# Kernel optimization log

Measured on AMD Instinct MI355X. Metric: run time of the kernel, lower is better.

Reference implementation:

```python
import jax, jax.numpy as jnp
import numpy as np

N_NODES = 100000
N_EDGES = 1600000
IN_DIM = 64
OUT_DIM = 64
BN_EPS = 1e-5


def batchnorm(h, gamma, beta):
    # BatchNorm1d in training mode: per-feature batch stats, biased variance
    mean = jnp.mean(h, axis=0)
    var = jnp.mean((h - mean) ** 2, axis=0)
    return gamma * (h - mean) * jax.lax.rsqrt(var + BN_EPS) + beta


def setup_inputs() -> dict:
    key = jax.random.key(0)
    ks = jax.random.split(key, 4)
    x = jax.random.normal(ks[0], (N_NODES, IN_DIM), dtype=jnp.float32)
    edge_index = jax.random.randint(ks[1], (2, N_EDGES), 0, N_NODES, dtype=jnp.int32)
    epsilon = jnp.asarray(0.1, dtype=jnp.float32)
    # Linear weights stored [in, out] (transpose of torch layout)
    W1 = jax.random.normal(ks[2], (IN_DIM, 2 * OUT_DIM), dtype=jnp.float32) * (1.0 / np.sqrt(IN_DIM))
    b1 = jnp.zeros((2 * OUT_DIM,), dtype=jnp.float32)
    g1 = jnp.ones((2 * OUT_DIM,), dtype=jnp.float32)
    be1 = jnp.zeros((2 * OUT_DIM,), dtype=jnp.float32)
    W2 = jax.random.normal(ks[3], (2 * OUT_DIM, OUT_DIM), dtype=jnp.float32) * (1.0 / np.sqrt(2 * OUT_DIM))
    b2 = jnp.zeros((OUT_DIM,), dtype=jnp.float32)
    g2 = jnp.ones((OUT_DIM,), dtype=jnp.float32)
    be2 = jnp.zeros((OUT_DIM,), dtype=jnp.float32)
    return {"x": x, "edge_index": edge_index, "epsilon": epsilon,
            "W1": W1, "b1": b1, "g1": g1, "be1": be1,
            "W2": W2, "b2": b2, "g2": g2, "be2": be2}


def reference(x, edge_index, epsilon, W1, b1, g1, be1, W2, b2, g2, be2):
    src, dst = edge_index[0], edge_index[1]
    # gather messages from src, scatter-add into dst  [N, D]
    neighbor_sum = jnp.zeros_like(x).at[dst].add(x[src])
    combined = (1.0 + epsilon) * x + neighbor_sum
    h = combined @ W1 + b1            # [N, 2*out_dim]
    h = jax.nn.relu(batchnorm(h, g1, be1))
    h = h @ W2 + b2                   # [N, out_dim]
    return batchnorm(h, g2, be2)
```

## Files before the change

kernel.cpp:

```cpp
#include <hip/hip_runtime.h>

#define N_NODES 100000
#define N_EDGES 1600000
#define IN_DIM 64
#define H_DIM 128
#define OUT_DIM 64
#define BN_EPS 1e-5f
#define CAP 64
#define BIN_SHIFT 9
#define BIN_NODES 512
#define NB 256
#define BINCAP 10240
#define NBIN_BLOCKS ((N_NODES + BIN_NODES - 1) / BIN_NODES)

#define OFF_XB     0
#define OFF_SRCL   3200000
#define OFF_BINNED 9600000
#define OFF_COMB   15000000
#define OFF_H1     18200000
#define OFF_H2     24600000
#define OFF_CNT    27800000
#define OFF_STATS  28000000
#define S1SUM 0
#define S1SQ  128
#define S2SUM 256
#define S2SQ  320

#define DEV_ATOMIC_ADD(p, v) __hip_atomic_fetch_add((p), (v), __ATOMIC_RELAXED, __HIP_MEMORY_SCOPE_AGENT)

typedef __attribute__((ext_vector_type(8))) short short8;
typedef __attribute__((ext_vector_type(4))) float f32x4;

__device__ __forceinline__ unsigned short f2bf(float f) {
  union { float f; unsigned u; } v; v.f = f;
  unsigned r = v.u + 0x7FFFu + ((v.u >> 16) & 1u);
  return (unsigned short)(r >> 16);
}
__device__ __forceinline__ float bflo(unsigned v) { union { unsigned u; float f; } t; t.u = v << 16; return t.f; }
__device__ __forceinline__ float bfhi(unsigned v) { union { unsigned u; float f; } t; t.u = v & 0xFFFF0000u; return t.f; }

__device__ __forceinline__ void acc8(float* a, uint4 v) {
  a[0] += bflo(v.x); a[1] += bfhi(v.x); a[2] += bflo(v.y); a[3] += bfhi(v.y);
  a[4] += bflo(v.z); a[5] += bfhi(v.z); a[6] += bflo(v.w); a[7] += bfhi(v.w);
}
__device__ __forceinline__ uint4 pack8(const float* a) {
  uint4 o;
  o.x = (unsigned)f2bf(a[0]) | ((unsigned)f2bf(a[1]) << 16);
  o.y = (unsigned)f2bf(a[2]) | ((unsigned)f2bf(a[3]) << 16);
  o.z = (unsigned)f2bf(a[4]) | ((unsigned)f2bf(a[5]) << 16);
  o.w = (unsigned)f2bf(a[6]) | ((unsigned)f2bf(a[7]) << 16);
  return o;
}

__global__ __launch_bounds__(256) void k_bsplit(const float* __restrict__ x,
                                                unsigned short* __restrict__ xb,
                                                const int* __restrict__ ei,
                                                int* __restrict__ bcnt,
                                                int2* __restrict__ binned) {
  __shared__ int lcnt[NB];
  __shared__ int lbase[NB];
  const int tid = threadIdx.x;
  lcnt[tid] = 0;
  #pragma unroll
  for (int j = 0; j < 8; ++j) {
    int i = blockIdx.x * 2048 + j * 256 + tid;
    if (i < N_NODES * IN_DIM / 4) {
      float4 v = ((const float4*)x)[i];
      ushort4 o;
      o.x = f2bf(v.x); o.y = f2bf(v.y); o.z = f2bf(v.z); o.w = f2bf(v.w);
      *(ushort4*)(xb + i * 4) = o;
    }
  }
  __syncthreads();
  int src[8], dst[8], rk[8];
  #pragma unroll
  for (int j = 0; j < 8; ++j) {
    int e = blockIdx.x * 2048 + j * 256 + tid;
    if (e < N_EDGES) {
      src[j] = ei[e];
      dst[j] = ei[N_EDGES + e];
      rk[j] = atomicAdd(&lcnt[dst[j] >> BIN_SHIFT], 1);
    } else {
      src[j] = -1;
    }
  }
  __syncthreads();
  if (lcnt[tid] > 0) lbase[tid] = DEV_ATOMIC_ADD(&bcnt[tid], lcnt[tid]);
  __syncthreads();
  #pragma unroll
  for (int j = 0; j < 8; ++j) {
    if (src[j] >= 0) {
      int b = dst[j] >> BIN_SHIFT;
      int pos = lbase[b] + rk[j];
      if (pos < BINCAP) binned[b * BINCAP + pos] = make_int2(src[j], dst[j]);
    }
  }
}

__global__ __launch_bounds__(512) void k_bfill(const int* __restrict__ bcnt,
                                               const int2* __restrict__ binned,
                                               int* __restrict__ cnt,
                                               int* __restrict__ srcl) {
  __shared__ int lcnt[BIN_NODES];
  const int tid = threadIdx.x;
  for (int i = tid; i < BIN_NODES; i += 512) lcnt[i] = 0;
  __syncthreads();
  const int b = blockIdx.x;
  int n = bcnt[b];
  if (n > BINCAP) n = BINCAP;
  const int2* run = binned + b * BINCAP;
  const int base = b * BIN_NODES;
  for (int i = tid; i < n; i += 512) {
    int2 ed = run[i];
    int pos = atomicAdd(&lcnt[ed.y - base], 1);
    if (pos < CAP) srcl[ed.y * CAP + pos] = ed.x;
  }
  __syncthreads();
  for (int i = tid; i < BIN_NODES; i += 512) {
    int node = base + i;
    if (node < N_NODES) cnt[node] = lcnt[i];
  }
}

__global__ __launch_bounds__(256, 5) void k_gather(const unsigned short* __restrict__ xb,
                                                   const float* __restrict__ eps,
                                                   const int* __restrict__ cnt,
                                                   const int* __restrict__ srcl,
                                                   unsigned short* __restrict__ comb) {
  const int t = blockIdx.x * 256 + threadIdx.x;
  const int node = t >> 3;
  const int sub = t & 7;
  if (node >= N_NODES) return;

  float a[8];
  {
    uint4 sv = *(const uint4*)(xb + node * 64 + sub * 8);
    float e1 = 1.0f + eps[0];
    a[0] = bflo(sv.x) * e1; a[1] = bfhi(sv.x) * e1;
    a[2] = bflo(sv.y) * e1; a[3] = bfhi(sv.y) * e1;
    a[4] = bflo(sv.z) * e1; a[5] = bfhi(sv.z) * e1;
    a[6] = bflo(sv.w) * e1; a[7] = bfhi(sv.w) * e1;
  }
  int deg = cnt[node];
  if (deg > CAP) deg = CAP;
  const int* sl = srcl + node * CAP;

  uint4 n0 = *(const uint4*)sl;
  uint4 n1 = *(const uint4*)(sl + 4);
  int j = 0;
  while (j + 8 <= deg) {
    uint4 i0 = n0, i1 = n1;
    uint4 r0 = *(const uint4*)(xb + (size_t)i0.x * 64 + sub * 8);
    uint4 r1 = *(const uint4*)(xb + (size_t)i0.y * 64 + sub * 8);
    uint4 r2 = *(const uint4*)(xb + (size_t)i0.z * 64 + sub * 8);
    uint4 r3 = *(const uint4*)(xb + (size_t)i0.w * 64 + sub * 8);
    uint4 r4 = *(const uint4*)(xb + (size_t)i1.x * 64 + sub * 8);
    uint4 r5 = *(const uint4*)(xb + (size_t)i1.y * 64 + sub * 8);
    uint4 r6 = *(const uint4*)(xb + (size_t)i1.z * 64 + sub * 8);
    uint4 r7 = *(const uint4*)(xb + (size_t)i1.w * 64 + sub * 8);
    j += 8;
    n0 = *(const uint4*)(sl + j);
    n1 = *(const uint4*)(sl + j + 4);
    acc8(a, r0); acc8(a, r1); acc8(a, r2); acc8(a, r3);
    acc8(a, r4); acc8(a, r5); acc8(a, r6); acc8(a, r7);
  }
  if (j + 4 <= deg) {
    uint4 i0 = *(const uint4*)(sl + j);
    uint4 r0 = *(const uint4*)(xb + (size_t)i0.x * 64 + sub * 8);
    uint4 r1 = *(const uint4*)(xb + (size_t)i0.y * 64 + sub * 8);
    uint4 r2 = *(const uint4*)(xb + (size_t)i0.z * 64 + sub * 8);
    uint4 r3 = *(const uint4*)(xb + (size_t)i0.w * 64 + sub * 8);
    acc8(a, r0); acc8(a, r1); acc8(a, r2); acc8(a, r3);
    j += 4;
  }
  if (j + 2 <= deg) {
    int2 i2 = *(const int2*)(sl + j);
    uint4 r0 = *(const uint4*)(xb + (size_t)i2.x * 64 + sub * 8);
    uint4 r1 = *(const uint4*)(xb + (size_t)i2.y * 64 + sub * 8);
    acc8(a, r0); acc8(a, r1);
    j += 2;
  }
  if (j < deg) {
    int s0 = sl[j];
    uint4 r0 = *(const uint4*)(xb + (size_t)s0 * 64 + sub * 8);
    acc8(a, r0);
  }
  *(uint4*)(comb + node * 64 + sub * 8) = pack8(a);
}

#define APAD 72
__global__ __launch_bounds__(256) void k_gemm1(const unsigned short* __restrict__ comb,
                                               const float* __restrict__ W1,
                                               const float* __restrict__ b1,
                                               unsigned short* __restrict__ h1,
                                               float* __restrict__ stats) {
  __shared__ unsigned short As[128 * APAD];
  __shared__ unsigned short Ws[128 * APAD];
  __shared__ float red[4][128];
  const int tid = threadIdx.x;
  const int wv = tid >> 6, lane = tid & 63;
  const int quad = lane >> 4, ln = lane & 15;
  const int rowBase = blockIdx.x * 128;

  #pragma unroll
  for (int it = 0; it < 8; ++it) {
    int idx = it * 256 + tid;
    int k = idx >> 5, n4 = idx & 31;
    float4 wv1 = *(const float4*)(W1 + k * 128 + n4 * 4);
    Ws[(n4 * 4 + 0) * APAD + k] = f2bf(wv1.x);
    Ws[(n4 * 4 + 1) * APAD + k] = f2bf(wv1.y);
    Ws[(n4 * 4 + 2) * APAD + k] = f2bf(wv1.z);
    Ws[(n4 * 4 + 3) * APAD + k] = f2bf(wv1.w);
  }
  #pragma unroll
  for (int it = 0; it < 4; ++it) {
    int idx = it * 256 + tid;
    int row = idx >> 3, ch = idx & 7;
    int g = rowBase * 8 + idx;
    uint4 u = (g < N_NODES * 8) ? ((const uint4*)comb)[g] : make_uint4(0, 0, 0, 0);
    *(uint4*)&As[row * APAD + ch * 8] = u;
  }
  __syncthreads();

  f32x4 acc[2][8];
  #pragma unroll
  for (int mt = 0; mt < 2; ++mt) {
    #pragma unroll
    for (int nt = 0; nt < 8; ++nt) acc[mt][nt] = (f32x4)0.0f;
  }
  const int rw = wv * 32;
  #pragma unroll
  for (int kb = 0; kb < 2; ++kb) {
    short8 a0 = *(short8*)&As[(rw + ln) * APAD + kb * 32 + quad * 8];
    short8 a1 = *(short8*)&As[(rw + 16 + ln) * APAD + kb * 32 + quad * 8];
    #pragma unroll
    for (int nt = 0; nt < 8; ++nt) {
      short8 b = *(short8*)&Ws[(nt * 16 + ln) * APAD + kb * 32 + quad * 8];
      acc[0][nt] = __builtin_amdgcn_mfma_f32_16x16x32_bf16(a0, b, acc[0][nt], 0, 0, 0);
      acc[1][nt] = __builtin_amdgcn_mfma_f32_16x16x32_bf16(a1, b, acc[1][nt], 0, 0, 0);
    }
  }

  float bias[8], s[8], q[8];
  #pragma unroll
  for (int nt = 0; nt < 8; ++nt) { bias[nt] = b1[nt * 16 + ln]; s[nt] = 0.f; q[nt] = 0.f; }
  #pragma unroll
  for (int mt = 0; mt < 2; ++mt) {
    #pragma unroll
    for (int i = 0; i < 4; ++i) {
      int gRow = rowBase + rw + mt * 16 + quad * 4 + i;
      if (gRow < N_NODES) {
        #pragma unroll
        for (int nt = 0; nt < 8; ++nt) {
          float v = acc[mt][nt][i] + bias[nt];
          h1[gRow * 128 + nt * 16 + ln] = f2bf(v);
          s[nt] += v; q[nt] += v * v;
        }
      }
    }
  }
  #pragma unroll
  for (int nt = 0; nt < 8; ++nt) {
    s[nt] += __shfl_xor(s[nt], 16); s[nt] += __shfl_xor(s[nt], 32);
    q[nt] += __shfl_xor(q[nt], 16); q[nt] += __shfl_xor(q[nt], 32);
  }
  if (lane < 16) {
    #pragma unroll
    for (int nt = 0; nt < 8; ++nt) red[wv][nt * 16 + ln] = s[nt];
  }
  __syncthreads();
  if (tid < 128) DEV_ATOMIC_ADD(&stats[S1SUM + tid],
                                red[0][tid] + red[1][tid] + red[2][tid] + red[3][tid]);
  __syncthreads();
  if (lane < 16) {
    #pragma unroll
    for (int nt = 0; nt < 8; ++nt) red[wv][nt * 16 + ln] = q[nt];
  }
  __syncthreads();
  if (tid < 128) DEV_ATOMIC_ADD(&stats[S1SQ + tid],
                                red[0][tid] + red[1][tid] + red[2][tid] + red[3][tid]);
}

#define WPAD 136
__global__ __launch_bounds__(256) void k_gemm2(const unsigned short* __restrict__ h1,
                                               const float* __restrict__ W2,
                                               const float* __restrict__ b2,
                                               const float* __restrict__ g1,
                                               const float* __restrict__ be1,
                                               unsigned short* __restrict__ h2,
                                               float* __restrict__ stats) {
  __shared__ unsigned short As[128 * APAD];
  __shared__ unsigned short Ws[64 * WPAD];
  __shared__ float red[4][64];
  __shared__ float scL[128], shL[128];
  const int tid = threadIdx.x;
  const int wv = tid >> 6, lane = tid & 63;
  const int quad = lane >> 4, ln = lane & 15;
  const int rowBase = blockIdx.x * 128;

  if (tid < 128) {
    float mean = stats[S1SUM + tid] * (1.0f / N_NODES);
    float var = stats[S1SQ + tid] * (1.0f / N_NODES) - mean * mean;
    var = fmaxf(var, 0.0f);
    float sc = g1[tid] * rsqrtf(var + BN_EPS);
    scL[tid] = sc;
    shL[tid] = be1[tid] - mean * sc;
  }
  #pragma unroll
  for (int it = 0; it < 8; ++it) {
    int idx = it * 256 + tid;
    int k = idx >> 4, n4 = idx & 15;
    float4 wv2 = *(const float4*)(W2 + k * 64 + n4 * 4);
    Ws[(n4 * 4 + 0) * WPAD + k] = f2bf(wv2.x);
    Ws[(n4 * 4 + 1) * WPAD + k] = f2bf(wv2.y);
    Ws[(n4 * 4 + 2) * WPAD + k] = f2bf(wv2.z);
    Ws[(n4 * 4 + 3) * WPAD + k] = f2bf(wv2.w);
  }

  f32x4 acc[2][4];
  #pragma unroll
  for (int mt = 0; mt < 2; ++mt) {
    #pragma unroll
    for (int nt = 0; nt < 4; ++nt) acc[mt][nt] = (f32x4)0.0f;
  }
  const int rw = wv * 32;

  for (int kc = 0; kc < 2; ++kc) {
    __syncthreads();
    #pragma unroll
    for (int it = 0; it < 4; ++it) {
      int idx = it * 256 + tid;
      int row = idx >> 3, ch = idx & 7;
      int gRow = rowBase + row;
      uint4 u = (gRow < N_NODES) ? *(const uint4*)(h1 + gRow * 128 + kc * 64 + ch * 8)
                                 : make_uint4(0, 0, 0, 0);
      int kb = kc * 64 + ch * 8;
      float f0 = fmaxf(bflo(u.x) * scL[kb + 0] + shL[kb + 0], 0.f);
      float f1 = fmaxf(bfhi(u.x) * scL[kb + 1] + shL[kb + 1], 0.f);
      float f2 = fmaxf(bflo(u.y) * scL[kb + 2] + shL[kb + 2], 0.f);
      float f3 = fmaxf(bfhi(u.y) * scL[kb + 3] + shL[kb + 3], 0.f);
      float f4 = fmaxf(bflo(u.z) * scL[kb + 4] + shL[kb + 4], 0.f);
      float f5 = fmaxf(bfhi(u.z) * scL[kb + 5] + shL[kb + 5], 0.f);
      float f6 = fmaxf(bflo(u.w) * scL[kb + 6] + shL[kb + 6], 0.f);
      float f7 = fmaxf(bfhi(u.w) * scL[kb + 7] + shL[kb + 7], 0.f);
      uint4 o;
      o.x = (unsigned)f2bf(f0) | ((unsigned)f2bf(f1) << 16);
      o.y = (unsigned)f2bf(f2) | ((unsigned)f2bf(f3) << 16);
      o.z = (unsigned)f2bf(f4) | ((unsigned)f2bf(f5) << 16);
      o.w = (unsigned)f2bf(f6) | ((unsigned)f2bf(f7) << 16);
      *(uint4*)&As[row * APAD + ch * 8] = o;
    }
    __syncthreads();
    #pragma unroll
    for (int kb = 0; kb < 2; ++kb) {
      short8 a0 = *(short8*)&As[(rw + ln) * APAD + kb * 32 + quad * 8];
      short8 a1 = *(short8*)&As[(rw + 16 + ln) * APAD + kb * 32 + quad * 8];
      #pragma unroll
      for (int nt = 0; nt < 4; ++nt) {
        short8 b = *(short8*)&Ws[(nt * 16 + ln) * WPAD + kc * 64 + kb * 32 + quad * 8];
        acc[0][nt] = __builtin_amdgcn_mfma_f32_16x16x32_bf16(a0, b, acc[0][nt], 0, 0, 0);
        acc[1][nt] = __builtin_amdgcn_mfma_f32_16x16x32_bf16(a1, b, acc[1][nt], 0, 0, 0);
      }
    }
  }

  float bias[4], s[4], q[4];
  #pragma unroll
  for (int nt = 0; nt < 4; ++nt) { bias[nt] = b2[nt * 16 + ln]; s[nt] = 0.f; q[nt] = 0.f; }
  #pragma unroll
  for (int mt = 0; mt < 2; ++mt) {
    #pragma unroll
    for (int i = 0; i < 4; ++i) {
      int gRow = rowBase + rw + mt * 16 + quad * 4 + i;
      if (gRow < N_NODES) {
        #pragma unroll
        for (int nt = 0; nt < 4; ++nt) {
          float v = acc[mt][nt][i] + bias[nt];
          h2[gRow * 64 + nt * 16 + ln] = f2bf(v);
          s[nt] += v; q[nt] += v * v;
        }
      }
    }
  }
  #pragma unroll
  for (int nt = 0; nt < 4; ++nt) {
    s[nt] += __shfl_xor(s[nt], 16); s[nt] += __shfl_xor(s[nt], 32);
    q[nt] += __shfl_xor(q[nt], 16); q[nt] += __shfl_xor(q[nt], 32);
  }
  if (lane < 16) {
    #pragma unroll
    for (int nt = 0; nt < 4; ++nt) red[wv][nt * 16 + ln] = s[nt];
  }
  __syncthreads();
  if (tid < 64) DEV_ATOMIC_ADD(&stats[S2SUM + tid],
                               red[0][tid] + red[1][tid] + red[2][tid] + red[3][tid]);
  __syncthreads();
  if (lane < 16) {
    #pragma unroll
    for (int nt = 0; nt < 4; ++nt) red[wv][nt * 16 + ln] = q[nt];
  }
  __syncthreads();
  if (tid < 64) DEV_ATOMIC_ADD(&stats[S2SQ + tid],
                               red[0][tid] + red[1][tid] + red[2][tid] + red[3][tid]);
}

__global__ __launch_bounds__(256) void k_out(const unsigned short* __restrict__ h2,
                                             const float* __restrict__ stats,
                                             const float* __restrict__ g2,
                                             const float* __restrict__ be2,
                                             float* __restrict__ out) {
  __shared__ float scL[64], shL[64];
  const int tid = threadIdx.x;
  if (tid < 64) {
    float mean = stats[S2SUM + tid] * (1.0f / N_NODES);
    float var = stats[S2SQ + tid] * (1.0f / N_NODES) - mean * mean;
    var = fmaxf(var, 0.0f);
    float sc = g2[tid] * rsqrtf(var + BN_EPS);
    scL[tid] = sc;
    shL[tid] = be2[tid] - mean * sc;
  }
  __syncthreads();
  int i = blockIdx.x * 256 + tid;
  if (i < N_NODES * OUT_DIM / 4) {
    int c = i & 15;
    uint2 u = *(const uint2*)(h2 + i * 4);
    float4 v = {bflo(u.x), bfhi(u.x), bflo(u.y), bfhi(u.y)};
    float4 sc = ((const float4*)scL)[c];
    float4 sh = ((const float4*)shL)[c];
    v.x = v.x * sc.x + sh.x;
    v.y = v.y * sc.y + sh.y;
    v.z = v.z * sc.z + sh.z;
    v.w = v.w * sc.w + sh.w;
    ((float4*)out)[i] = v;
  }
}

extern "C" void kernel_launch(void* const* d_in, const int* in_sizes, int n_in,
                              void* d_out, int out_size, void* d_ws, size_t ws_size,
                              hipStream_t stream) {
  const float* x   = (const float*)d_in[0];
  const int*   ei  = (const int*)d_in[1];
  const float* eps = (const float*)d_in[2];
  const float* W1  = (const float*)d_in[3];
  const float* b1  = (const float*)d_in[4];
  const float* g1  = (const float*)d_in[5];
  const float* be1 = (const float*)d_in[6];
  const float* W2  = (const float*)d_in[7];
  const float* b2  = (const float*)d_in[8];
  const float* g2  = (const float*)d_in[9];
  const float* be2 = (const float*)d_in[10];

  float* ws = (float*)d_ws;
  unsigned short* xb     = (unsigned short*)(ws + OFF_XB);
  int*            srcl   = (int*)(ws + OFF_SRCL);
  int2*           binned = (int2*)(ws + OFF_BINNED);
  unsigned short* comb   = (unsigned short*)(ws + OFF_COMB);
  unsigned short* h1     = (unsigned short*)(ws + OFF_H1);
  unsigned short* h2     = (unsigned short*)(ws + OFF_H2);
  int*            cnt    = (int*)(ws + OFF_CNT);
  float*          stats  = ws + OFF_STATS;
  int*            bcnt   = (int*)(stats + 768);
  float*          out    = (float*)d_out;

  hipMemsetAsync(stats, 0, 1024 * sizeof(float), stream);

  const int edgeGrid = (N_EDGES + 2047) / 2048;
  const int gemmGrid = (N_NODES + 127) / 128;
  const int gatherGrid = (N_NODES * 8 + 255) / 256;
  k_bsplit<<<edgeGrid, 256, 0, stream>>>(x, xb, ei, bcnt, binned);
  k_bfill<<<NBIN_BLOCKS, 512, 0, stream>>>(bcnt, binned, cnt, srcl);
  k_gather<<<gatherGrid, 256, 0, stream>>>(xb, eps, cnt, srcl, comb);
  k_gemm1<<<gemmGrid, 256, 0, stream>>>(comb, W1, b1, h1, stats);
  k_gemm2<<<gemmGrid, 256, 0, stream>>>(h1, W2, b2, g1, be1, h2, stats);
  k_out<<<(N_NODES * OUT_DIM / 4 + 255) / 256, 256, 0, stream>>>(h2, stats, g2, be2, out);
}
```

Measured before the change: 239.2 us.

## Replace binned two-pass adjacency build with direct global atomic fill

Removes the bin-split and bin-fill kernels that staged edges by destination bucket using shared-memory atomics. Edges are now inserted directly into per-node source lists using device-scope atomic counters on a zeroed count array. This drops one kernel launch and the intermediate binned edge buffer, but replaces local atomics and grouped writes with random global atomics and scattered stores. It also adds a memset for the count array.

```diff
diff --git a/kernel.cpp b/kernel.cpp
--- a/kernel.cpp
+++ b/kernel.cpp
@@ -7,20 +7,14 @@
 #define OUT_DIM 64
 #define BN_EPS 1e-5f
 #define CAP 64
-#define BIN_SHIFT 9
-#define BIN_NODES 512
-#define NB 256
-#define BINCAP 10240
-#define NBIN_BLOCKS ((N_NODES + BIN_NODES - 1) / BIN_NODES)
 
 #define OFF_XB     0
 #define OFF_SRCL   3200000
-#define OFF_BINNED 9600000
-#define OFF_COMB   15000000
-#define OFF_H1     18200000
-#define OFF_H2     24600000
-#define OFF_CNT    27800000
-#define OFF_STATS  28000000
+#define OFF_COMB   9600000
+#define OFF_H1     12800000
+#define OFF_H2     19200000
+#define OFF_CNT    22400000
+#define OFF_STATS  22600000
 #define S1SUM 0
 #define S1SQ  128
 #define S2SUM 256
@@ -52,15 +46,12 @@
   return o;
 }
 
-__global__ __launch_bounds__(256) void k_bsplit(const float* __restrict__ x,
-                                                unsigned short* __restrict__ xb,
-                                                const int* __restrict__ ei,
-                                                int* __restrict__ bcnt,
-                                                int2* __restrict__ binned) {
-  __shared__ int lcnt[NB];
-  __shared__ int lbase[NB];
+__global__ __launch_bounds__(256) void k_build(const float* __restrict__ x,
+                                               unsigned short* __restrict__ xb,
+                                               const int* __restrict__ ei,
+                                               int* __restrict__ cnt,
+                                               int* __restrict__ srcl) {
   const int tid = threadIdx.x;
-  lcnt[tid] = 0;
   #pragma unroll
   for (int j = 0; j < 8; ++j) {
     int i = blockIdx.x * 2048 + j * 256 + tid;
@@ -71,54 +62,15 @@
       *(ushort4*)(xb + i * 4) = o;
     }
   }
-  __syncthreads();
-  int src[8], dst[8], rk[8];
   #pragma unroll
   for (int j = 0; j < 8; ++j) {
     int e = blockIdx.x * 2048 + j * 256 + tid;
     if (e < N_EDGES) {
-      src[j] = ei[e];
-      dst[j] = ei[N_EDGES + e];
-      rk[j] = atomicAdd(&lcnt[dst[j] >> BIN_SHIFT], 1);
-    } else {
-      src[j] = -1;
-    }
-  }
-  __syncthreads();
-  if (lcnt[tid] > 0) lbase[tid] = DEV_ATOMIC_ADD(&bcnt[tid], lcnt[tid]);
-  __syncthreads();
-  #pragma unroll
-  for (int j = 0; j < 8; ++j) {
-    if (src[j] >= 0) {
-      int b = dst[j] >> BIN_SHIFT;
-      int pos = lbase[b] + rk[j];
-      if (pos < BINCAP) binned[b * BINCAP + pos] = make_int2(src[j], dst[j]);
-    }
-  }
-}
-
-__global__ __launch_bounds__(512) void k_bfill(const int* __restrict__ bcnt,
-                                               const int2* __restrict__ binned,
-                                               int* __restrict__ cnt,
-                                               int* __restrict__ srcl) {
-  __shared__ int lcnt[BIN_NODES];
-  const int tid = threadIdx.x;
-  for (int i = tid; i < BIN_NODES; i += 512) lcnt[i] = 0;
-  __syncthreads();
-  const int b = blockIdx.x;
-  int n = bcnt[b];
-  if (n > BINCAP) n = BINCAP;
-  const int2* run = binned + b * BINCAP;
-  const int base = b * BIN_NODES;
-  for (int i = tid; i < n; i += 512) {
-    int2 ed = run[i];
-    int pos = atomicAdd(&lcnt[ed.y - base], 1);
-    if (pos < CAP) srcl[ed.y * CAP + pos] = ed.x;
-  }
-  __syncthreads();
-  for (int i = tid; i < BIN_NODES; i += 512) {
-    int node = base + i;
-    if (node < N_NODES) cnt[node] = lcnt[i];
+      int src = ei[e];
+      int dst = ei[N_EDGES + e];
+      int pos = DEV_ATOMIC_ADD(&cnt[dst], 1);
+      if (pos < CAP) srcl[dst * CAP + pos] = src;
+    }
   }
 }
 
@@ -453,22 +405,20 @@
   float* ws = (float*)d_ws;
   unsigned short* xb     = (unsigned short*)(ws + OFF_XB);
   int*            srcl   = (int*)(ws + OFF_SRCL);
-  int2*           binned = (int2*)(ws + OFF_BINNED);
   unsigned short* comb   = (unsigned short*)(ws + OFF_COMB);
   unsigned short* h1     = (unsigned short*)(ws + OFF_H1);
   unsigned short* h2     = (unsigned short*)(ws + OFF_H2);
   int*            cnt    = (int*)(ws + OFF_CNT);
   float*          stats  = ws + OFF_STATS;
-  int*            bcnt   = (int*)(stats + 768);
   float*          out    = (float*)d_out;
 
-  hipMemsetAsync(stats, 0, 1024 * sizeof(float), stream);
+  hipMemsetAsync(stats, 0, 768 * sizeof(float), stream);
+  hipMemsetAsync(cnt, 0, N_NODES * sizeof(int), stream);
 
   const int edgeGrid = (N_EDGES + 2047) / 2048;
   const int gemmGrid = (N_NODES + 127) / 128;
   const int gatherGrid = (N_NODES * 8 + 255) / 256;
-  k_bsplit<<<edgeGrid, 256, 0, stream>>>(x, xb, ei, bcnt, binned);
-  k_bfill<<<NBIN_BLOCKS, 512, 0, stream>>>(bcnt, binned, cnt, srcl);
+  k_build<<<edgeGrid, 256, 0, stream>>>(x, xb, ei, cnt, srcl);
   k_gather<<<gatherGrid, 256, 0, stream>>>(xb, eps, cnt, srcl, comb);
   k_gemm1<<<gemmGrid, 256, 0, stream>>>(comb, W1, b1, h1, stats);
   k_gemm2<<<gemmGrid, 256, 0, stream>>>(h1, W2, b2, g1, be1, h2, stats);
```

New measurement: 335.2 us. 40.1% more time.

## Pack binned edges into single ints and split gather across two thread groups

Applied to the files above, without the earlier changes.

Binned edge records shrink from int2 (src, dst) to a single packed int holding the source index and the local destination offset, which halves the binning write and read traffic. The gather kernel now gives each node 16 threads in two groups that take alternating 4-edge chunks and combine their partial sums with a cross-lane shuffle. This doubles parallelism and memory-level concurrency per node, at the cost of twice as many threads and a redundant count load per group. The occupancy hint rises to 6 blocks per SM. The packing relies on src << 9 fitting in an int, which holds for 100k nodes.

```diff
diff --git a/kernel.cpp b/kernel.cpp
--- a/kernel.cpp
+++ b/kernel.cpp
@@ -56,7 +56,7 @@
                                                 unsigned short* __restrict__ xb,
                                                 const int* __restrict__ ei,
                                                 int* __restrict__ bcnt,
-                                                int2* __restrict__ binned) {
+                                                int* __restrict__ binned) {
   __shared__ int lcnt[NB];
   __shared__ int lbase[NB];
   const int tid = threadIdx.x;
@@ -92,13 +92,14 @@
     if (src[j] >= 0) {
       int b = dst[j] >> BIN_SHIFT;
       int pos = lbase[b] + rk[j];
-      if (pos < BINCAP) binned[b * BINCAP + pos] = make_int2(src[j], dst[j]);
+      if (pos < BINCAP)
+        binned[b * BINCAP + pos] = (src[j] << BIN_SHIFT) | (dst[j] & (BIN_NODES - 1));
     }
   }
 }
 
 __global__ __launch_bounds__(512) void k_bfill(const int* __restrict__ bcnt,
-                                               const int2* __restrict__ binned,
+                                               const int* __restrict__ binned,
                                                int* __restrict__ cnt,
                                                int* __restrict__ srcl) {
   __shared__ int lcnt[BIN_NODES];
@@ -108,12 +109,13 @@
   const int b = blockIdx.x;
   int n = bcnt[b];
   if (n > BINCAP) n = BINCAP;
-  const int2* run = binned + b * BINCAP;
+  const int* run = binned + b * BINCAP;
   const int base = b * BIN_NODES;
   for (int i = tid; i < n; i += 512) {
-    int2 ed = run[i];
-    int pos = atomicAdd(&lcnt[ed.y - base], 1);
-    if (pos < CAP) srcl[ed.y * CAP + pos] = ed.x;
+    int p = run[i];
+    int lid = p & (BIN_NODES - 1);
+    int pos = atomicAdd(&lcnt[lid], 1);
+    if (pos < CAP) srcl[(base + lid) * CAP + pos] = p >> BIN_SHIFT;
   }
   __syncthreads();
   for (int i = tid; i < BIN_NODES; i += 512) {
@@ -122,18 +124,23 @@
   }
 }
 
-__global__ __launch_bounds__(256, 5) void k_gather(const unsigned short* __restrict__ xb,
+__global__ __launch_bounds__(256, 6) void k_gather(const unsigned short* __restrict__ xb,
                                                    const float* __restrict__ eps,
                                                    const int* __restrict__ cnt,
                                                    const int* __restrict__ srcl,
                                                    unsigned short* __restrict__ comb) {
   const int t = blockIdx.x * 256 + threadIdx.x;
-  const int node = t >> 3;
+  const int node = t >> 4;
+  const int g = (t >> 3) & 1;
   const int sub = t & 7;
   if (node >= N_NODES) return;
 
+  const unsigned short* xs = xb + sub * 8;
   float a[8];
-  {
+  #pragma unroll
+  for (int i = 0; i < 8; ++i) a[i] = 0.f;
+
+  if (g == 0) {
     uint4 sv = *(const uint4*)(xb + node * 64 + sub * 8);
     float e1 = 1.0f + eps[0];
     a[0] = bflo(sv.x) * e1; a[1] = bfhi(sv.x) * e1;
@@ -145,47 +152,40 @@
   if (deg > CAP) deg = CAP;
   const int* sl = srcl + node * CAP;
 
-  uint4 n0 = *(const uint4*)sl;
-  uint4 n1 = *(const uint4*)(sl + 4);
-  int j = 0;
-  while (j + 8 <= deg) {
-    uint4 i0 = n0, i1 = n1;
-    uint4 r0 = *(const uint4*)(xb + (size_t)i0.x * 64 + sub * 8);
-    uint4 r1 = *(const uint4*)(xb + (size_t)i0.y * 64 + sub * 8);
-    uint4 r2 = *(const uint4*)(xb + (size_t)i0.z * 64 + sub * 8);
-    uint4 r3 = *(const uint4*)(xb + (size_t)i0.w * 64 + sub * 8);
-    uint4 r4 = *(const uint4*)(xb + (size_t)i1.x * 64 + sub * 8);
-    uint4 r5 = *(const uint4*)(xb + (size_t)i1.y * 64 + sub * 8);
-    uint4 r6 = *(const uint4*)(xb + (size_t)i1.z * 64 + sub * 8);
-    uint4 r7 = *(const uint4*)(xb + (size_t)i1.w * 64 + sub * 8);
-    j += 8;
-    n0 = *(const uint4*)(sl + j);
-    n1 = *(const uint4*)(sl + j + 4);
+  int j = g * 4;
+  while (j + 12 <= deg) {
+    uint4 i0 = *(const uint4*)(sl + j);
+    uint4 i1 = *(const uint4*)(sl + j + 8);
+    uint4 r0 = *(const uint4*)(xs + (size_t)i0.x * 64);
+    uint4 r1 = *(const uint4*)(xs + (size_t)i0.y * 64);
+    uint4 r2 = *(const uint4*)(xs + (size_t)i0.z * 64);
+    uint4 r3 = *(const uint4*)(xs + (size_t)i0.w * 64);
+    uint4 r4 = *(const uint4*)(xs + (size_t)i1.x * 64);
+    uint4 r5 = *(const uint4*)(xs + (size_t)i1.y * 64);
+    uint4 r6 = *(const uint4*)(xs + (size_t)i1.z * 64);
+    uint4 r7 = *(const uint4*)(xs + (size_t)i1.w * 64);
     acc8(a, r0); acc8(a, r1); acc8(a, r2); acc8(a, r3);
     acc8(a, r4); acc8(a, r5); acc8(a, r6); acc8(a, r7);
+    j += 16;
   }
   if (j + 4 <= deg) {
     uint4 i0 = *(const uint4*)(sl + j);
-    uint4 r0 = *(const uint4*)(xb + (size_t)i0.x * 64 + sub * 8);
-    uint4 r1 = *(const uint4*)(xb + (size_t)i0.y * 64 + sub * 8);
-    uint4 r2 = *(const uint4*)(xb + (size_t)i0.z * 64 + sub * 8);
-    uint4 r3 = *(const uint4*)(xb + (size_t)i0.w * 64 + sub * 8);
+    uint4 r0 = *(const uint4*)(xs + (size_t)i0.x * 64);
+    uint4 r1 = *(const uint4*)(xs + (size_t)i0.y * 64);
+    uint4 r2 = *(const uint4*)(xs + (size_t)i0.z * 64);
+    uint4 r3 = *(const uint4*)(xs + (size_t)i0.w * 64);
     acc8(a, r0); acc8(a, r1); acc8(a, r2); acc8(a, r3);
-    j += 4;
-  }
-  if (j + 2 <= deg) {
-    int2 i2 = *(const int2*)(sl + j);
-    uint4 r0 = *(const uint4*)(xb + (size_t)i2.x * 64 + sub * 8);
-    uint4 r1 = *(const uint4*)(xb + (size_t)i2.y * 64 + sub * 8);
-    acc8(a, r0); acc8(a, r1);
-    j += 2;
-  }
-  if (j < deg) {
-    int s0 = sl[j];
-    uint4 r0 = *(const uint4*)(xb + (size_t)s0 * 64 + sub * 8);
-    acc8(a, r0);
-  }
-  *(uint4*)(comb + node * 64 + sub * 8) = pack8(a);
+  }
+  if (g == ((deg >> 2) & 1)) {
+    for (int k = deg & ~3; k < deg; ++k) {
+      int s0 = sl[k];
+      uint4 r = *(const uint4*)(xs + (size_t)s0 * 64);
+      acc8(a, r);
+    }
+  }
+  #pragma unroll
+  for (int i = 0; i < 8; ++i) a[i] += __shfl_xor(a[i], 8);
+  if (g == 0) *(uint4*)(comb + node * 64 + sub * 8) = pack8(a);
 }
 
 #define APAD 72
@@ -453,7 +453,7 @@
   float* ws = (float*)d_ws;
   unsigned short* xb     = (unsigned short*)(ws + OFF_XB);
   int*            srcl   = (int*)(ws + OFF_SRCL);
-  int2*           binned = (int2*)(ws + OFF_BINNED);
+  int*            binned = (int*)(ws + OFF_BINNED);
   unsigned short* comb   = (unsigned short*)(ws + OFF_COMB);
   unsigned short* h1     = (unsigned short*)(ws + OFF_H1);
   unsigned short* h2     = (unsigned short*)(ws + OFF_H2);
@@ -466,7 +466,7 @@
 
   const int edgeGrid = (N_EDGES + 2047) / 2048;
   const int gemmGrid = (N_NODES + 127) / 128;
-  const int gatherGrid = (N_NODES * 8 + 255) / 256;
+  const int gatherGrid = (N_NODES * 16 + 255) / 256;
   k_bsplit<<<edgeGrid, 256, 0, stream>>>(x, xb, ei, bcnt, binned);
   k_bfill<<<NBIN_BLOCKS, 512, 0, stream>>>(bcnt, binned, cnt, srcl);
   k_gather<<<gatherGrid, 256, 0, stream>>>(xb, eps, cnt, srcl, comb);
```

Result: no change. 237.5 us (-0.7%).
